# Kernel optimization log

Measured on AMD Instinct MI355X. Metric: run time of the kernel, lower is better.

Reference implementation:

```python
import jax, jax.numpy as jnp
import numpy as np

DIM = 96
HEADS = 3
HEAD_DIM = DIM // HEADS
WIN = (4, 4, 4)
N_WIN = WIN[0] * WIN[1] * WIN[2]  # 64 tokens per window
HIDDEN = int(DIM * 4.0)
EPS = 1e-5


def setup_inputs() -> dict:
    key = jax.random.key(0)
    ks = jax.random.split(key, 16)
    s = lambda fan: 1.0 / np.sqrt(fan)
    return {
        "x": jax.random.normal(ks[0], (1, 64, 96, 96, 96), jnp.float32),
        "g1": jnp.ones((DIM,), jnp.float32),
        "b1": jnp.zeros((DIM,), jnp.float32),
        "wq": jax.random.normal(ks[1], (DIM, DIM), jnp.float32) * s(DIM),
        "bq": jnp.zeros((DIM,), jnp.float32),
        "wkv": jax.random.normal(ks[2], (DIM, 2 * DIM), jnp.float32) * s(DIM),
        "bkv": jnp.zeros((2 * DIM,), jnp.float32),
        "wp": jax.random.normal(ks[3], (DIM, DIM), jnp.float32) * s(DIM),
        "bp": jnp.zeros((DIM,), jnp.float32),
        "g2": jnp.ones((DIM,), jnp.float32),
        "b2": jnp.zeros((DIM,), jnp.float32),
        "w1": jax.random.normal(ks[4], (DIM, HIDDEN), jnp.float32) * s(DIM),
        "bm1": jnp.zeros((HIDDEN,), jnp.float32),
        "w2": jax.random.normal(ks[5], (HIDDEN, DIM), jnp.float32) * s(HIDDEN),
        "bm2": jnp.zeros((DIM,), jnp.float32),
    }


def _layernorm(x, g, b):
    mu = jnp.mean(x, axis=-1, keepdims=True)
    var = jnp.mean(jnp.square(x - mu), axis=-1, keepdims=True)
    return (x - mu) * jax.lax.rsqrt(var + EPS) * g + b


def _window_partition(x):
    B, D, H, W, C = x.shape
    wd, wh, ww = WIN
    x = x.reshape(B, D // wd, wd, H // wh, wh, W // ww, ww, C)
    x = x.transpose(0, 1, 3, 5, 2, 4, 6, 7)
    return x.reshape(-1, N_WIN, C)


def _window_reverse(win, B, D, H, W):
    wd, wh, ww = WIN
    C = win.shape[-1]
    x = win.reshape(B, D // wd, H // wh, W // ww, wd, wh, ww, C)
    x = x.transpose(0, 1, 4, 2, 5, 3, 6, 7)
    return x.reshape(B, D, H, W, C)


def reference(x, g1, b1, wq, bq, wkv, bkv, wp, bp, g2, b2, w1, bm1, w2, bm2):
    B, D, H, W, C = x.shape
    # --- part 1: LN -> window attention -> residual ---
    h = _layernorm(x, g1, b1)
    # D,H,W chosen divisible by window size, so padding is a no-op
    xw = _window_partition(h)                       # (nW, N, C)
    nW = xw.shape[0]
    q = (xw @ wq + bq).reshape(nW, N_WIN, HEADS, HEAD_DIM)
    kv = (xw @ wkv + bkv).reshape(nW, N_WIN, 2, HEADS, HEAD_DIM)
    k, v = kv[:, :, 0], kv[:, :, 1]                 # (nW, N, h, hd)
    scale = HEAD_DIM ** -0.5
    attn = jnp.einsum("wnhd,wmhd->whnm", q * scale, k)
    attn = jax.nn.softmax(attn, axis=-1)
    out = jnp.einsum("whnm,wmhd->wnhd", attn, v).reshape(nW, N_WIN, C)
    out = out @ wp + bp
    attn_out = _window_reverse(out, B, D, H, W)
    x = x + attn_out
    # --- part 2: LN -> MLP -> residual ---
    h2 = _layernorm(x, g2, b2)
    h2 = jax.nn.gelu(h2 @ w1 + bm1, approximate=False) @ w2 + bm2
    return x + h2
```

## Files before the change

kernel.cpp:

```cpp
#include <hip/hip_runtime.h>

typedef __bf16 bf16x8 __attribute__((ext_vector_type(8)));
typedef __bf16 bf16x4 __attribute__((ext_vector_type(4)));
typedef float f32x4 __attribute__((ext_vector_type(4)));

#define MFMA(a,b,c) __builtin_amdgcn_mfma_f32_16x16x32_bf16(a, b, c, 0, 0, 0)

__device__ __forceinline__ float gelu_f(float t) {
    float t2 = t * t;
    float m = t * __builtin_fmaf(-0.07135481627f, t2, -1.5957691216f);
    float e = __expf(m);
    return t * __builtin_amdgcn_rcpf(1.0f + e);
}

__device__ __forceinline__ bf16x4 shfl_b4(bf16x4 v, int srcLane) {
    union { bf16x4 b; int i[2]; } u; u.b = v;
    u.i[0] = __shfl(u.i[0], srcLane);
    u.i[1] = __shfl(u.i[1], srcLane);
    return u.b;
}
__device__ __forceinline__ bf16x8 frag_from_packs(const bf16x4* pk, int m, int g, int c) {
    int l_lo = c + 32 * (g & 1);
    int l_hi = l_lo + 16;
    bf16x4 a0 = shfl_b4(pk[2*m],   l_lo);
    bf16x4 a1 = shfl_b4(pk[2*m+1], l_lo);
    bf16x4 b0 = shfl_b4(pk[2*m],   l_hi);
    bf16x4 b1 = shfl_b4(pk[2*m+1], l_hi);
    bool sel = ((g >> 1) & 1);
    bf16x4 lo = sel ? a1 : a0;
    bf16x4 hi = sel ? b1 : b0;
    bf16x8 r;
    #pragma unroll
    for (int i = 0; i < 4; ++i) { r[i] = lo[i]; r[i+4] = hi[i]; }
    return r;
}

__global__ void prep_weights(const float* __restrict__ wq, const float* __restrict__ wkv,
                             const float* __restrict__ wp, const float* __restrict__ w1,
                             const float* __restrict__ w2, __bf16* __restrict__ ws) {
    int i = blockIdx.x * 256 + threadIdx.x;
    const float scale = 0.17677669529663687f;
    if (i < 9216) {
        int n = i / 96, k = i % 96;
        ws[i] = (__bf16)(wq[k * 96 + n] * scale);
    } else if (i < 27648) {
        int j = i - 9216; int n = j / 96, k = j % 96;
        ws[i] = (__bf16)(wkv[k * 192 + n]);
    } else if (i < 36864) {
        int j = i - 27648; int n = j / 96, k = j % 96;
        ws[i] = (__bf16)(wp[k * 96 + n]);
    } else if (i < 73728) {
        int j = i - 36864; int n = j / 96, k = j % 96;
        ws[i] = (__bf16)(w1[k * 384 + n]);
    } else if (i < 110592) {
        int j = i - 73728; int n = j / 384, k = j % 384;
        ws[i] = (__bf16)(w2[k * 96 + n]);
    }
}

#define LDH 104
#define LDV 72

#define AOFF_H   0
#define AOFF_Q   6656
#define AOFF_K   13312
#define AOFF_VT  19968
#define ASMEM    26880

__global__ __launch_bounds__(256, 2) void attn_kernel(
    const float* __restrict__ x, const float* __restrict__ g1v, const float* __restrict__ b1v,
    const float* __restrict__ bq, const float* __restrict__ bkv, const float* __restrict__ bp,
    const __bf16* __restrict__ ws, float* __restrict__ xmid)
{
    const __bf16* wqt  = ws;
    const __bf16* wkvt = ws + 9216;
    const __bf16* wpt  = ws + 27648;

    __shared__ __align__(16) __bf16 smem[ASMEM];
    __bf16* h_lds  = smem + AOFF_H;
    __bf16* q_lds  = smem + AOFF_Q;
    __bf16* k_lds  = smem + AOFF_K;
    __bf16* vt_lds = smem + AOFF_VT;

    const int tid = threadIdx.x;
    const int wv = tid >> 6, lane = tid & 63;
    const int c = lane & 15, g = lane >> 4;

    const int wid = blockIdx.x;
    const int wdI = wid / 576, rem = wid % 576, whI = rem / 24, wwI = rem % 24;
    const int tok = tid >> 2, cseg = (tid & 3) * 24;
    const int dz = tok >> 4, hy = (tok >> 2) & 3, wx = tok & 3;
    const long gbase = (((long)(wdI * 4 + dz) * 96 + (whI * 4 + hy)) * 96 + (wwI * 4 + wx)) * 96 + cseg;

    const f32x4 fzero = {0.f, 0.f, 0.f, 0.f};

    float xr[24];
    #pragma unroll
    for (int j = 0; j < 6; ++j) {
        float4 v = *reinterpret_cast<const float4*>(x + gbase + j * 4);
        xr[j*4+0] = v.x; xr[j*4+1] = v.y; xr[j*4+2] = v.z; xr[j*4+3] = v.w;
    }
    {
        float s = 0.f;
        #pragma unroll
        for (int j = 0; j < 24; ++j) s += xr[j];
        s += __shfl_xor(s, 1); s += __shfl_xor(s, 2);
        float mu = s * (1.0f / 96.0f);
        float vs = 0.f;
        #pragma unroll
        for (int j = 0; j < 24; ++j) { float d = xr[j] - mu; vs += d * d; }
        vs += __shfl_xor(vs, 1); vs += __shfl_xor(vs, 2);
        float rstd = rsqrtf(vs * (1.0f / 96.0f) + 1e-5f);
        #pragma unroll
        for (int j = 0; j < 6; ++j) {
            f32x4 gv = *reinterpret_cast<const f32x4*>(g1v + cseg + j * 4);
            f32x4 bv = *reinterpret_cast<const f32x4*>(b1v + cseg + j * 4);
            bf16x4 o;
            #pragma unroll
            for (int r = 0; r < 4; ++r) o[r] = (__bf16)((xr[j*4+r] - mu) * rstd * gv[r] + bv[r]);
            *reinterpret_cast<bf16x4*>(&h_lds[tok * LDH + cseg + j*4]) = o;
        }
    }
    __syncthreads();

    {
        bf16x8 bH[3];
        #pragma unroll
        for (int kc = 0; kc < 3; ++kc)
            bH[kc] = *reinterpret_cast<const bf16x8*>(&h_lds[(wv*16 + c) * LDH + kc*32 + g*8]);
        f32x4 aq[6];
        #pragma unroll
        for (int nt = 0; nt < 6; ++nt) aq[nt] = fzero;
        #pragma unroll
        for (int nt = 0; nt < 6; ++nt)
            #pragma unroll
            for (int kc = 0; kc < 3; ++kc) {
                bf16x8 aW = *reinterpret_cast<const bf16x8*>(&wqt[(nt*16 + c) * 96 + kc*32 + g*8]);
                aq[nt] = MFMA(aW, bH[kc], aq[nt]);
            }
        #pragma unroll
        for (int nt = 0; nt < 6; ++nt) {
            f32x4 bb = *reinterpret_cast<const f32x4*>(&bq[nt*16 + 4*g]);
            bf16x4 o;
            #pragma unroll
            for (int r = 0; r < 4; ++r) o[r] = (__bf16)(aq[nt][r] + bb[r] * 0.17677669529663687f);
            *reinterpret_cast<bf16x4*>(&q_lds[(wv*16 + c) * LDH + nt*16 + 4*g]) = o;
        }
    }
    if (wv < 2) {
        #pragma unroll
        for (int t2 = 0; t2 < 2; ++t2) {
            int tt = wv*2 + t2;
            bf16x8 bH[3];
            #pragma unroll
            for (int kc = 0; kc < 3; ++kc)
                bH[kc] = *reinterpret_cast<const bf16x8*>(&h_lds[(tt*16 + c) * LDH + kc*32 + g*8]);
            f32x4 ak[6];
            #pragma unroll
            for (int nt = 0; nt < 6; ++nt) ak[nt] = fzero;
            #pragma unroll
            for (int nt = 0; nt < 6; ++nt)
                #pragma unroll
                for (int kc = 0; kc < 3; ++kc) {
                    bf16x8 aW = *reinterpret_cast<const bf16x8*>(&wkvt[(nt*16 + c) * 96 + kc*32 + g*8]);
                    ak[nt] = MFMA(aW, bH[kc], ak[nt]);
                }
            #pragma unroll
            for (int nt = 0; nt < 6; ++nt) {
                f32x4 bb = *reinterpret_cast<const f32x4*>(&bkv[nt*16 + 4*g]);
                bf16x4 o;
                #pragma unroll
                for (int r = 0; r < 4; ++r) o[r] = (__bf16)(ak[nt][r] + bb[r]);
                *reinterpret_cast<bf16x4*>(&k_lds[(tt*16 + c) * LDH + nt*16 + 4*g]) = o;
            }
        }
    } else {
        f32x4 av[4][3];
        #pragma unroll
        for (int m = 0; m < 4; ++m)
            #pragma unroll
            for (int nl = 0; nl < 3; ++nl) av[m][nl] = fzero;
        #pragma unroll
        for (int kc = 0; kc < 3; ++kc) {
            bf16x8 aH[4];
            #pragma unroll
            for (int m = 0; m < 4; ++m)
                aH[m] = *reinterpret_cast<const bf16x8*>(&h_lds[(m*16 + c) * LDH + kc*32 + g*8]);
            #pragma unroll
            for (int nl = 0; nl < 3; ++nl) {
                int nv = (wv - 2) * 3 + nl;
                bf16x8 bW = *reinterpret_cast<const bf16x8*>(&wkvt[(96 + nv*16 + c) * 96 + kc*32 + g*8]);
                #pragma unroll
                for (int m = 0; m < 4; ++m)
                    av[m][nl] = MFMA(aH[m], bW, av[m][nl]);
            }
        }
        #pragma unroll
        for (int nl = 0; nl < 3; ++nl) {
            int nv = (wv - 2) * 3 + nl;
            float bias = bkv[96 + nv*16 + c];
            #pragma unroll
            for (int m = 0; m < 4; ++m) {
                bf16x4 o;
                #pragma unroll
                for (int r = 0; r < 4; ++r) o[r] = (__bf16)(av[m][nl][r] + bias);
                *reinterpret_cast<bf16x4*>(&vt_lds[(nv*16 + c) * LDV + m*16 + 4*g]) = o;
            }
        }
    }
    __syncthreads();

    #pragma unroll
    for (int h = 0; h < 3; ++h) {
        f32x4 sacc[4];
        bf16x8 bQ = *reinterpret_cast<const bf16x8*>(&q_lds[(wv*16 + c) * LDH + h*32 + g*8]);
        #pragma unroll
        for (int nt = 0; nt < 4; ++nt) {
            bf16x8 aK = *reinterpret_cast<const bf16x8*>(&k_lds[(nt*16 + c) * LDH + h*32 + g*8]);
            sacc[nt] = fzero;
            sacc[nt] = MFMA(aK, bQ, sacc[nt]);
        }
        float mx = sacc[0][0];
        #pragma unroll
        for (int nt = 0; nt < 4; ++nt)
            #pragma unroll
            for (int r = 0; r < 4; ++r) mx = fmaxf(mx, sacc[nt][r]);
        mx = fmaxf(mx, __shfl_xor(mx, 16));
        mx = fmaxf(mx, __shfl_xor(mx, 32));
        float p[4][4]; float se = 0.f;
        #pragma unroll
        for (int nt = 0; nt < 4; ++nt)
            #pragma unroll
            for (int r = 0; r < 4; ++r) { p[nt][r] = __expf(sacc[nt][r] - mx); se += p[nt][r]; }
        se += __shfl_xor(se, 16);
        se += __shfl_xor(se, 32);
        float rsinv = __builtin_amdgcn_rcpf(se);
        bf16x4 pp[4];
        #pragma unroll
        for (int nt = 0; nt < 4; ++nt)
            #pragma unroll
            for (int r = 0; r < 4; ++r) pp[nt][r] = (__bf16)p[nt][r];

        f32x4 oacc[2];
        oacc[0] = fzero;
        oacc[1] = fzero;
        #pragma unroll
        for (int kc = 0; kc < 2; ++kc) {
            bf16x8 bP = frag_from_packs(pp, kc, g, c);
            #pragma unroll
            for (int n2 = 0; n2 < 2; ++n2) {
                bf16x8 aV = *reinterpret_cast<const bf16x8*>(&vt_lds[(h*32 + n2*16 + c) * LDV + kc*32 + g*8]);
                oacc[n2] = MFMA(aV, bP, oacc[n2]);
            }
        }
        #pragma unroll
        for (int n2 = 0; n2 < 2; ++n2) {
            bf16x4 o;
            #pragma unroll
            for (int r = 0; r < 4; ++r) o[r] = (__bf16)(oacc[n2][r] * rsinv);
            *reinterpret_cast<bf16x4*>(&h_lds[(wv*16 + c) * LDH + h*32 + n2*16 + 4*g]) = o;
        }
    }

    {
        bf16x8 bA[3];
        #pragma unroll
        for (int kc = 0; kc < 3; ++kc)
            bA[kc] = *reinterpret_cast<const bf16x8*>(&h_lds[(wv*16 + c) * LDH + kc*32 + g*8]);
        f32x4 ap[6];
        #pragma unroll
        for (int nt = 0; nt < 6; ++nt) ap[nt] = fzero;
        #pragma unroll
        for (int nt = 0; nt < 6; ++nt)
            #pragma unroll
            for (int kc = 0; kc < 3; ++kc) {
                bf16x8 aW = *reinterpret_cast<const bf16x8*>(&wpt[(nt*16 + c) * 96 + kc*32 + g*8]);
                ap[nt] = MFMA(aW, bA[kc], ap[nt]);
            }
        #pragma unroll
        for (int nt = 0; nt < 6; ++nt) {
            f32x4 bb = *reinterpret_cast<const f32x4*>(&bp[nt*16 + 4*g]);
            bf16x4 o;
            #pragma unroll
            for (int r = 0; r < 4; ++r) o[r] = (__bf16)(ap[nt][r] + bb[r]);
            *reinterpret_cast<bf16x4*>(&q_lds[(wv*16 + c) * LDH + nt*16 + 4*g]) = o;
        }
    }

    #pragma unroll
    for (int j = 0; j < 6; ++j) {
        bf16x4 pr = *reinterpret_cast<const bf16x4*>(&q_lds[tok * LDH + cseg + j*4]);
        float4 v;
        v.x = xr[j*4+0] + (float)pr[0];
        v.y = xr[j*4+1] + (float)pr[1];
        v.z = xr[j*4+2] + (float)pr[2];
        v.w = xr[j*4+3] + (float)pr[3];
        *reinterpret_cast<float4*>(xmid + gbase + j * 4) = v;
    }
}

#define LDU 104
#define LDC2 104

__global__ __launch_bounds__(384, 4) void mlp_kernel(
    float* __restrict__ xio, const float* __restrict__ g2v, const float* __restrict__ b2v,
    const float* __restrict__ bm1, const float* __restrict__ bm2,
    const __bf16* __restrict__ ws)
{
    const __bf16* w1t = ws + 36864;
    const __bf16* w2t = ws + 73728;

    __shared__ __align__(16) __bf16 u_lds[64 * LDU];
    __shared__ __align__(16) __bf16 hid[64 * LDC2];

    const int tid = threadIdx.x;
    const int wv = tid >> 6, lane = tid & 63;
    const int c = lane & 15, g = lane >> 4;

    const int tok = tid >> 2, cseg = (tid & 3) * 24;
    const long gaddr = ((long)blockIdx.x * 64 + tok) * 96 + cseg;

    const f32x4 fzero = {0.f, 0.f, 0.f, 0.f};

    if (tid < 256) {
        float xr[24];
        #pragma unroll
        for (int j = 0; j < 6; ++j) {
            float4 v = *reinterpret_cast<const float4*>(xio + gaddr + j * 4);
            xr[j*4+0] = v.x; xr[j*4+1] = v.y; xr[j*4+2] = v.z; xr[j*4+3] = v.w;
        }
        float s = 0.f;
        #pragma unroll
        for (int j = 0; j < 24; ++j) s += xr[j];
        s += __shfl_xor(s, 1); s += __shfl_xor(s, 2);
        float mu = s * (1.0f / 96.0f);
        float vs = 0.f;
        #pragma unroll
        for (int j = 0; j < 24; ++j) { float d = xr[j] - mu; vs += d * d; }
        vs += __shfl_xor(vs, 1); vs += __shfl_xor(vs, 2);
        float rstd = rsqrtf(vs * (1.0f / 96.0f) + 1e-5f);
        #pragma unroll
        for (int j = 0; j < 6; ++j) {
            f32x4 gv = *reinterpret_cast<const f32x4*>(g2v + cseg + j * 4);
            f32x4 bv = *reinterpret_cast<const f32x4*>(b2v + cseg + j * 4);
            bf16x4 o;
            #pragma unroll
            for (int r = 0; r < 4; ++r) o[r] = (__bf16)((xr[j*4+r] - mu) * rstd * gv[r] + bv[r]);
            *reinterpret_cast<bf16x4*>(&u_lds[tok * LDU + cseg + j*4]) = o;
        }
    }
    __syncthreads();

    f32x4 accB[4];
    #pragma unroll
    for (int tt = 0; tt < 4; ++tt) accB[tt] = fzero;

    #pragma unroll
    for (int ch = 0; ch < 4; ++ch) {
        f32x4 accA[4];
        #pragma unroll
        for (int tt = 0; tt < 4; ++tt) accA[tt] = fzero;
        #pragma unroll
        for (int kc = 0; kc < 3; ++kc) {
            bf16x8 aW = *reinterpret_cast<const bf16x8*>(&w1t[((ch*6 + wv)*16 + c) * 96 + kc*32 + g*8]);
            #pragma unroll
            for (int tt = 0; tt < 4; ++tt) {
                bf16x8 bU = *reinterpret_cast<const bf16x8*>(&u_lds[(tt*16 + c) * LDU + kc*32 + g*8]);
                accA[tt] = MFMA(aW, bU, accA[tt]);
            }
        }
        {
            f32x4 bb = *reinterpret_cast<const f32x4*>(&bm1[(ch*6 + wv)*16 + 4*g]);
            #pragma unroll
            for (int tt = 0; tt < 4; ++tt) {
                bf16x4 o;
                #pragma unroll
                for (int r = 0; r < 4; ++r) o[r] = (__bf16)gelu_f(accA[tt][r] + bb[r]);
                *reinterpret_cast<bf16x4*>(&hid[(tt*16 + c) * LDC2 + wv*16 + 4*g]) = o;
            }
        }
        __syncthreads();

        #pragma unroll
        for (int kc = 0; kc < 3; ++kc) {
            bf16x8 aW2 = *reinterpret_cast<const bf16x8*>(&w2t[(wv*16 + c) * 384 + ch*96 + kc*32 + g*8]);
            #pragma unroll
            for (int tt = 0; tt < 4; ++tt) {
                bf16x8 bHd = *reinterpret_cast<const bf16x8*>(&hid[(tt*16 + c) * LDC2 + kc*32 + g*8]);
                accB[tt] = MFMA(aW2, bHd, accB[tt]);
            }
        }
        if (ch < 3) __syncthreads();
    }

    {
        f32x4 bb = *reinterpret_cast<const f32x4*>(&bm2[wv*16 + 4*g]);
        #pragma unroll
        for (int tt = 0; tt < 4; ++tt) {
            bf16x4 o;
            #pragma unroll
            for (int r = 0; r < 4; ++r) o[r] = (__bf16)(accB[tt][r] + bb[r]);
            *reinterpret_cast<bf16x4*>(&u_lds[(tt*16 + c) * LDU + wv*16 + 4*g]) = o;
        }
    }
    __syncthreads();

    if (tid < 256) {
        #pragma unroll
        for (int j = 0; j < 6; ++j) {
            float4 xv = *reinterpret_cast<const float4*>(xio + gaddr + j * 4);
            bf16x4 mo = *reinterpret_cast<const bf16x4*>(&u_lds[tok * LDU + cseg + j*4]);
            float4 v;
            v.x = xv.x + (float)mo[0];
            v.y = xv.y + (float)mo[1];
            v.z = xv.z + (float)mo[2];
            v.w = xv.w + (float)mo[3];
            *reinterpret_cast<float4*>(xio + gaddr + j * 4) = v;
        }
    }
}

extern "C" void kernel_launch(void* const* d_in, const int* in_sizes, int n_in,
                              void* d_out, int out_size, void* d_ws, size_t ws_size,
                              hipStream_t stream) {
    (void)in_sizes; (void)n_in; (void)out_size; (void)ws_size;
    const float* x   = (const float*)d_in[0];
    const float* g1  = (const float*)d_in[1];
    const float* b1  = (const float*)d_in[2];
    const float* wq  = (const float*)d_in[3];
    const float* bq  = (const float*)d_in[4];
    const float* wkv = (const float*)d_in[5];
    const float* bkv = (const float*)d_in[6];
    const float* wp  = (const float*)d_in[7];
    const float* bp  = (const float*)d_in[8];
    const float* g2  = (const float*)d_in[9];
    const float* b2  = (const float*)d_in[10];
    const float* w1  = (const float*)d_in[11];
    const float* bm1 = (const float*)d_in[12];
    const float* w2  = (const float*)d_in[13];
    const float* bm2 = (const float*)d_in[14];
    float* out = (float*)d_out;
    __bf16* ws = (__bf16*)d_ws;

    prep_weights<<<432, 256, 0, stream>>>(wq, wkv, wp, w1, w2, ws);
    attn_kernel<<<9216, 256, 0, stream>>>(x, g1, b1, bq, bkv, bp, ws, out);
    mlp_kernel<<<9216, 384, 0, stream>>>(out, g2, b2, bm1, bm2, ws);
}
```

Measured before the change: 498.3 us.

## Give each wave its own token rows for QKV, keep Q in registers

```diff
diff --git a/kernel.cpp b/kernel.cpp
--- a/kernel.cpp
+++ b/kernel.cpp
@@ -62,12 +62,11 @@
 #define LDV 72
 
 #define AOFF_H   0
-#define AOFF_Q   6656
-#define AOFF_K   13312
-#define AOFF_VT  19968
-#define ASMEM    26880
-
-__global__ __launch_bounds__(256, 2) void attn_kernel(
+#define AOFF_K   6656
+#define AOFF_VT  13312
+#define ASMEM    20224
+
+__global__ __launch_bounds__(256, 4) void attn_kernel(
     const float* __restrict__ x, const float* __restrict__ g1v, const float* __restrict__ b1v,
     const float* __restrict__ bq, const float* __restrict__ bkv, const float* __restrict__ bp,
     const __bf16* __restrict__ ws, float* __restrict__ xmid)
@@ -78,7 +77,6 @@
 
     __shared__ __align__(16) __bf16 smem[ASMEM];
     __bf16* h_lds  = smem + AOFF_H;
-    __bf16* q_lds  = smem + AOFF_Q;
     __bf16* k_lds  = smem + AOFF_K;
     __bf16* vt_lds = smem + AOFF_VT;
 
@@ -121,13 +119,14 @@
             *reinterpret_cast<bf16x4*>(&h_lds[tok * LDH + cseg + j*4]) = o;
         }
     }
-    __syncthreads();
-
-    {
-        bf16x8 bH[3];
-        #pragma unroll
-        for (int kc = 0; kc < 3; ++kc)
-            bH[kc] = *reinterpret_cast<const bf16x8*>(&h_lds[(wv*16 + c) * LDH + kc*32 + g*8]);
+
+    bf16x8 bH[3];
+    #pragma unroll
+    for (int kc = 0; kc < 3; ++kc)
+        bH[kc] = *reinterpret_cast<const bf16x8*>(&h_lds[(wv*16 + c) * LDH + kc*32 + g*8]);
+
+    bf16x4 qp[6];
+    {
         f32x4 aq[6];
         #pragma unroll
         for (int nt = 0; nt < 6; ++nt) aq[nt] = fzero;
@@ -141,79 +140,57 @@
         #pragma unroll
         for (int nt = 0; nt < 6; ++nt) {
             f32x4 bb = *reinterpret_cast<const f32x4*>(&bq[nt*16 + 4*g]);
-            bf16x4 o;
-            #pragma unroll
-            for (int r = 0; r < 4; ++r) o[r] = (__bf16)(aq[nt][r] + bb[r] * 0.17677669529663687f);
-            *reinterpret_cast<bf16x4*>(&q_lds[(wv*16 + c) * LDH + nt*16 + 4*g]) = o;
-        }
-    }
-    if (wv < 2) {
-        #pragma unroll
-        for (int t2 = 0; t2 < 2; ++t2) {
-            int tt = wv*2 + t2;
-            bf16x8 bH[3];
-            #pragma unroll
-            for (int kc = 0; kc < 3; ++kc)
-                bH[kc] = *reinterpret_cast<const bf16x8*>(&h_lds[(tt*16 + c) * LDH + kc*32 + g*8]);
-            f32x4 ak[6];
-            #pragma unroll
-            for (int nt = 0; nt < 6; ++nt) ak[nt] = fzero;
-            #pragma unroll
-            for (int nt = 0; nt < 6; ++nt)
-                #pragma unroll
-                for (int kc = 0; kc < 3; ++kc) {
-                    bf16x8 aW = *reinterpret_cast<const bf16x8*>(&wkvt[(nt*16 + c) * 96 + kc*32 + g*8]);
-                    ak[nt] = MFMA(aW, bH[kc], ak[nt]);
-                }
-            #pragma unroll
-            for (int nt = 0; nt < 6; ++nt) {
-                f32x4 bb = *reinterpret_cast<const f32x4*>(&bkv[nt*16 + 4*g]);
-                bf16x4 o;
-                #pragma unroll
-                for (int r = 0; r < 4; ++r) o[r] = (__bf16)(ak[nt][r] + bb[r]);
-                *reinterpret_cast<bf16x4*>(&k_lds[(tt*16 + c) * LDH + nt*16 + 4*g]) = o;
-            }
-        }
-    } else {
-        f32x4 av[4][3];
-        #pragma unroll
-        for (int m = 0; m < 4; ++m)
-            #pragma unroll
-            for (int nl = 0; nl < 3; ++nl) av[m][nl] = fzero;
+            #pragma unroll
+            for (int r = 0; r < 4; ++r) qp[nt][r] = (__bf16)(aq[nt][r] + bb[r] * 0.17677669529663687f);
+        }
+    }
+    {
+        f32x4 ak[6];
+        #pragma unroll
+        for (int nt = 0; nt < 6; ++nt) ak[nt] = fzero;
+        #pragma unroll
+        for (int nt = 0; nt < 6; ++nt)
+            #pragma unroll
+            for (int kc = 0; kc < 3; ++kc) {
+                bf16x8 aW = *reinterpret_cast<const bf16x8*>(&wkvt[(nt*16 + c) * 96 + kc*32 + g*8]);
+                ak[nt] = MFMA(aW, bH[kc], ak[nt]);
+            }
+        #pragma unroll
+        for (int nt = 0; nt < 6; ++nt) {
+            f32x4 bb = *reinterpret_cast<const f32x4*>(&bkv[nt*16 + 4*g]);
+            bf16x4 o;
+            #pragma unroll
+            for (int r = 0; r < 4; ++r) o[r] = (__bf16)(ak[nt][r] + bb[r]);
+            *reinterpret_cast<bf16x4*>(&k_lds[(wv*16 + c) * LDH + nt*16 + 4*g]) = o;
+        }
+    }
+    {
+        f32x4 av[6];
+        #pragma unroll
+        for (int nv = 0; nv < 6; ++nv) av[nv] = fzero;
         #pragma unroll
         for (int kc = 0; kc < 3; ++kc) {
-            bf16x8 aH[4];
-            #pragma unroll
-            for (int m = 0; m < 4; ++m)
-                aH[m] = *reinterpret_cast<const bf16x8*>(&h_lds[(m*16 + c) * LDH + kc*32 + g*8]);
-            #pragma unroll
-            for (int nl = 0; nl < 3; ++nl) {
-                int nv = (wv - 2) * 3 + nl;
+            #pragma unroll
+            for (int nv = 0; nv < 6; ++nv) {
                 bf16x8 bW = *reinterpret_cast<const bf16x8*>(&wkvt[(96 + nv*16 + c) * 96 + kc*32 + g*8]);
-                #pragma unroll
-                for (int m = 0; m < 4; ++m)
-                    av[m][nl] = MFMA(aH[m], bW, av[m][nl]);
-            }
-        }
-        #pragma unroll
-        for (int nl = 0; nl < 3; ++nl) {
-            int nv = (wv - 2) * 3 + nl;
+                av[nv] = MFMA(bH[kc], bW, av[nv]);
+            }
+        }
+        #pragma unroll
+        for (int nv = 0; nv < 6; ++nv) {
             float bias = bkv[96 + nv*16 + c];
-            #pragma unroll
-            for (int m = 0; m < 4; ++m) {
-                bf16x4 o;
-                #pragma unroll
-                for (int r = 0; r < 4; ++r) o[r] = (__bf16)(av[m][nl][r] + bias);
-                *reinterpret_cast<bf16x4*>(&vt_lds[(nv*16 + c) * LDV + m*16 + 4*g]) = o;
-            }
+            bf16x4 o;
+            #pragma unroll
+            for (int r = 0; r < 4; ++r) o[r] = (__bf16)(av[nv][r] + bias);
+            *reinterpret_cast<bf16x4*>(&vt_lds[(nv*16 + c) * LDV + wv*16 + 4*g]) = o;
         }
     }
     __syncthreads();
 
     #pragma unroll
     for (int h = 0; h < 3; ++h) {
+        bf16x8 bQ = frag_from_packs(qp, h, g, c);
         f32x4 sacc[4];
-        bf16x8 bQ = *reinterpret_cast<const bf16x8*>(&q_lds[(wv*16 + c) * LDH + h*32 + g*8]);
         #pragma unroll
         for (int nt = 0; nt < 4; ++nt) {
             bf16x8 aK = *reinterpret_cast<const bf16x8*>(&k_lds[(nt*16 + c) * LDH + h*32 + g*8]);
@@ -261,6 +238,7 @@
             *reinterpret_cast<bf16x4*>(&h_lds[(wv*16 + c) * LDH + h*32 + n2*16 + 4*g]) = o;
         }
     }
+    __syncthreads();
 
     {
         bf16x8 bA[3];
@@ -283,13 +261,13 @@
             bf16x4 o;
             #pragma unroll
             for (int r = 0; r < 4; ++r) o[r] = (__bf16)(ap[nt][r] + bb[r]);
-            *reinterpret_cast<bf16x4*>(&q_lds[(wv*16 + c) * LDH + nt*16 + 4*g]) = o;
+            *reinterpret_cast<bf16x4*>(&k_lds[(wv*16 + c) * LDH + nt*16 + 4*g]) = o;
         }
     }
 
     #pragma unroll
     for (int j = 0; j < 6; ++j) {
-        bf16x4 pr = *reinterpret_cast<const bf16x4*>(&q_lds[tok * LDH + cseg + j*4]);
+        bf16x4 pr = *reinterpret_cast<const bf16x4*>(&k_lds[tok * LDH + cseg + j*4]);
         float4 v;
         v.x = xr[j*4+0] + (float)pr[0];
         v.y = xr[j*4+1] + (float)pr[1];
```

After: 517.6 us. +3.9%, slower.
